# Kernel optimization log

Hardware: AMD Instinct MI355X
Metric: run time of the kernel (lower is better)

The kernel has to match this reference:

```python
import jax, jax.numpy as jnp
import numpy as np

HIDDEN_DIM = 2048
HEAD_NUM = 16
HEAD_DIM = HIDDEN_DIM // HEAD_NUM


def setup_inputs() -> dict:
    key = jax.random.key(0)
    ks = jax.random.split(key, 9)
    B, S, H = 2, 2048, HIDDEN_DIM
    scale = 1.0 / np.sqrt(H)
    X = jax.random.normal(ks[0], (B, S, H), dtype=jnp.float32)
    Wq = jax.random.normal(ks[1], (H, H), dtype=jnp.float32) * scale
    bq = jnp.zeros((H,), dtype=jnp.float32)
    Wk = jax.random.normal(ks[2], (H, H), dtype=jnp.float32) * scale
    bk = jnp.zeros((H,), dtype=jnp.float32)
    Wv = jax.random.normal(ks[3], (H, H), dtype=jnp.float32) * scale
    bv = jnp.zeros((H,), dtype=jnp.float32)
    Wo = jax.random.normal(ks[4], (H, H), dtype=jnp.float32) * scale
    bo = jnp.zeros((H,), dtype=jnp.float32)
    return {"X": X, "Wq": Wq, "bq": bq, "Wk": Wk, "bk": bk,
            "Wv": Wv, "bv": bv, "Wo": Wo, "bo": bo}


def reference(X, Wq, bq, Wk, bk, Wv, bv, Wo, bo):
    B, S, H = X.shape
    # QKV projections (nn.Linear applies x @ W.T + b; weights here stored as [in, out])
    Q = X @ Wq + bq
    K = X @ Wk + bk
    V = X @ Wv + bv
    # [B, heads, S, head_dim]
    q = Q.reshape(B, S, HEAD_NUM, HEAD_DIM).transpose(0, 2, 1, 3)
    k = K.reshape(B, S, HEAD_NUM, HEAD_DIM).transpose(0, 2, 1, 3)
    v = V.reshape(B, S, HEAD_NUM, HEAD_DIM).transpose(0, 2, 1, 3)
    scores = jnp.einsum('bhqd,bhkd->bhqk', q, k) / jnp.sqrt(jnp.float32(HEAD_DIM))
    attn = jax.nn.softmax(scores, axis=-1)  # dropout = identity in eval
    out = jnp.einsum('bhqk,bhkd->bhqd', attn, v)
    out = out.transpose(0, 2, 1, 3).reshape(B, S, H)
    return out @ Wo + bo
```

## Files before the change

### kernel.cpp

```cpp
#include <hip/hip_runtime.h>
#include <hip/hip_bf16.h>
#include <stdint.h>


#define Bc 2
#define Sc 2048
#define Hc 2048
#define NHc 16
#define Dc 128
#define Mc 4096

typedef unsigned short ushortT;
typedef float f32x4 __attribute__((ext_vector_type(4)));
typedef _Float16 f16x8 __attribute__((ext_vector_type(8)));

#define MFMAH(a, b, c) __builtin_amdgcn_mfma_f32_16x16x32_f16((a), (b), (c), 0, 0, 0)

static __device__ __forceinline__ ushortT f2h(float x) {
    _Float16 h = (_Float16)x;
    return __builtin_bit_cast(unsigned short, h);
}

static __device__ __forceinline__ void load_lds16(const ushortT* g, ushortT* l) {
    __builtin_amdgcn_global_load_lds(
        (__attribute__((address_space(1))) void*)(g),
        (__attribute__((address_space(3))) void*)(l), 16, 0, 0);
}

__global__ __launch_bounds__(256) void pack_a(
    const float* __restrict__ src, ushortT* __restrict__ dst)
{
    const int mt = blockIdx.x, kt = blockIdx.y;
    const int t = threadIdx.x;
    const int kq = t & 15;
    const int r0 = t >> 4;
    ushortT* tile = dst + ((size_t)(mt * 32 + kt)) * 8192;
#pragma unroll
    for (int rr = 0; rr < 8; ++rr) {
        const int row = r0 + rr * 16;
        const float4 v = *(const float4*)(src + (size_t)(mt * 128 + row) * Hc + kt * 64 + kq * 4);
        _Float16 h[4] = {(_Float16)v.x, (_Float16)v.y, (_Float16)v.z, (_Float16)v.w};
        const int gid = kq >> 1, halfg = kq & 1;
        const int gp = gid ^ (row & 7);
        *(uint2*)(tile + (size_t)row * 64 + gp * 8 + halfg * 4) = *(uint2*)h;
    }
}

__global__ __launch_bounds__(256) void pack_b(
    const float* __restrict__ W0, const float* __restrict__ W1,
    const float* __restrict__ W2, const float* __restrict__ W3,
    ushortT* __restrict__ dst)
{
    const int nt = blockIdx.x, kt = blockIdx.y, which = blockIdx.z;
    const float* W = (which == 0) ? W0 : (which == 1) ? W1 : (which == 2) ? W2 : W3;
    const int t = threadIdx.x;
    const int n = t & 127;
    const int g0 = (t >> 7) * 4;
    ushortT* tile = dst + (size_t)which * 4194304 + ((size_t)(nt * 32 + kt)) * 8192;
#pragma unroll
    for (int gi = 0; gi < 4; ++gi) {
        const int g = g0 + gi;
        _Float16 h[8];
#pragma unroll
        for (int j = 0; j < 8; ++j)
            h[j] = (_Float16)W[(size_t)(kt * 64 + g * 8 + j) * Hc + nt * 128 + n];
        const int gp = g ^ (n & 7);
        *(uint4*)(tile + (size_t)n * 64 + gp * 8) = *(uint4*)h;
    }
}

#define G256_PROLOGUE()                                                        \
    __shared__ __align__(16) ushortT LA[2][2][8192];                           \
    __shared__ __align__(16) ushortT LB[2][2][8192];                           \
    const int tid = threadIdx.x, wv_ = tid >> 6, lane = tid & 63;              \
    const int lane16 = lane & 15, quad = lane >> 4, quad4 = (lane >> 4) * 4;   \
    const int wr = wv_ >> 2, wc = wv_ & 3;                                     \
    f32x4 acc[8][4];                                                           \
    _Pragma("unroll") for (int i = 0; i < 8; ++i)                              \
        _Pragma("unroll") for (int j = 0; j < 4; ++j) {                        \
            acc[i][j][0] = 0.f; acc[i][j][1] = 0.f;                            \
            acc[i][j][2] = 0.f; acc[i][j][3] = 0.f; }

#define STAGE(GT, LDST) do {                                                   \
    const ushortT* g_ = (GT) + wv_ * 1024 + lane * 8;                          \
    ushortT* l_ = (LDST) + wv_ * 1024;                                         \
    load_lds16(g_, l_);                                                        \
    load_lds16(g_ + 512, l_ + 512);                                            \
} while (0)

#define RD_A(S, RB)                                                            \
    _Pragma("unroll") for (int mi = 0; mi < 4; ++mi) {                         \
        const int r_ = (RB) + mi * 16 + lane16;                                \
        _Pragma("unroll") for (int kf = 0; kf < 2; ++kf)                       \
            a[mi][kf] = *(const f16x8*)&LA[S][wr][r_ * 64 +                    \
                (((kf * 4 + quad) ^ (r_ & 7)) << 3)];                          \
    }

#define RD_B(S)                                                                \
    _Pragma("unroll") for (int nj = 0; nj < 4; ++nj) {                         \
        const int r_ = (wc & 1) * 64 + nj * 16 + lane16;                       \
        _Pragma("unroll") for (int kf = 0; kf < 2; ++kf)                       \
            b[nj][kf] = *(const f16x8*)&LB[S][wc >> 1][r_ * 64 +               \
                (((kf * 4 + quad) ^ (r_ & 7)) << 3)];                          \
    }

#define QUAD(MIB, NJB)                                                         \
    _Pragma("unroll") for (int kf = 0; kf < 2; ++kf)                           \
        _Pragma("unroll") for (int mi = 0; mi < 4; ++mi)                       \
            _Pragma("unroll") for (int nj = 0; nj < 2; ++nj)                   \
                acc[(MIB) + mi][(NJB) + nj] =                                  \
                    MFMAH(a[mi][kf], b[(NJB) + nj][kf], acc[(MIB) + mi][(NJB) + nj]);

#define PRE_MFMA()                                                             \
    __builtin_amdgcn_sched_barrier(0);                                         \
    __builtin_amdgcn_s_barrier();                                              \
    __builtin_amdgcn_sched_barrier(0);                                         \
    __builtin_amdgcn_s_setprio(1);

#define POST_MFMA()                                                            \
    __builtin_amdgcn_s_setprio(0);                                             \
    __builtin_amdgcn_sched_barrier(0);                                         \
    __builtin_amdgcn_s_barrier();                                              \
    __builtin_amdgcn_sched_barrier(0);

#define VMC6() asm volatile("s_waitcnt vmcnt(6)" ::: "memory")

#define MINS(x) ((x) < 31 ? (x) : 31)

#define G256_MAIN(AB0, AB1, BB0, BB1)                                          \
      \
    STAGE(BB0, &LB[0][0][0]); STAGE(BB1, &LB[0][1][0]);                        \
    STAGE(AB0, &LA[0][0][0]); STAGE(AB1, &LA[0][1][0]);                        \
    STAGE(BB0 + 8192, &LB[1][0][0]); STAGE(BB1 + 8192, &LB[1][1][0]);          \
    STAGE(AB0 + 8192, &LA[1][0][0]);                                           \
    VMC6();                                                                    \
    __builtin_amdgcn_sched_barrier(0);                                         \
    __builtin_amdgcn_s_barrier();                                              \
    __builtin_amdgcn_sched_barrier(0);                                         \
    _Pragma("clang loop unroll(disable)")                                      \
    for (int t = 0; t < 32; t += 2) {                                          \
        f16x8 a[4][2], b[4][2];                                                \
                                \
        RD_A(0, 0); RD_B(0);                                                   \
        STAGE(AB1 + (size_t)(t + 1) * 8192, &LA[1][1][0]);                     \
        PRE_MFMA(); QUAD(0, 0); POST_MFMA();                                   \
                                            \
        STAGE(BB0 + (size_t)MINS(t + 2) * 8192, &LB[0][0][0]);                 \
        PRE_MFMA(); QUAD(0, 2); POST_MFMA();                                   \
                                                       \
        RD_A(0, 64);                                                           \
        STAGE(BB1 + (size_t)MINS(t + 2) * 8192, &LB[0][1][0]);                 \
        PRE_MFMA(); QUAD(4, 2); POST_MFMA();                                   \
            \
        STAGE(AB0 + (size_t)MINS(t + 2) * 8192, &LA[0][0][0]);                 \
        VMC6();                                                                \
        PRE_MFMA(); QUAD(4, 0); POST_MFMA();                                   \
                                             \
        RD_A(1, 0); RD_B(1);                                                   \
        STAGE(AB1 + (size_t)MINS(t + 2) * 8192, &LA[0][1][0]);                 \
        PRE_MFMA(); QUAD(0, 0); POST_MFMA();                                   \
                                                                       \
        STAGE(BB0 + (size_t)MINS(t + 3) * 8192, &LB[1][0][0]);                 \
        PRE_MFMA(); QUAD(0, 2); POST_MFMA();                                   \
                                                                       \
        RD_A(1, 64);                                                           \
        STAGE(BB1 + (size_t)MINS(t + 3) * 8192, &LB[1][1][0]);                 \
        PRE_MFMA(); QUAD(4, 2); POST_MFMA();                                   \
                            \
        STAGE(AB0 + (size_t)MINS(t + 3) * 8192, &LA[1][0][0]);                 \
        VMC6();                                                                \
        PRE_MFMA(); QUAD(4, 0); POST_MFMA();                                   \
    }

__global__ __launch_bounds__(512, 2) void qkv_gemm256(
    const ushortT* __restrict__ Xp, const ushortT* __restrict__ Wall,
    const float* __restrict__ bq, const float* __restrict__ bk,
    const float* __restrict__ bv,
    ushortT* __restrict__ Qd, ushortT* __restrict__ Kd, ushortT* __restrict__ Vt)
{
    const int id = blockIdx.x;
    const int swz = (id & 7) * 48 + (id >> 3);
    const int mt = swz & 15;
    const int bn = swz >> 4;
    const int which = bn >> 3, bnw = bn & 7;
    const ushortT* Ab0 = Xp + (size_t)((2 * mt + 0) * 32) * 8192;
    const ushortT* Ab1 = Xp + (size_t)((2 * mt + 1) * 32) * 8192;
    const ushortT* Wp  = Wall + (size_t)which * 4194304;
    const ushortT* Bb0 = Wp + (size_t)((bnw * 2 + 0) * 32) * 8192;
    const ushortT* Bb1 = Wp + (size_t)((bnw * 2 + 1) * 32) * 8192;
    const float* bias = (which == 0) ? bq : (which == 1) ? bk : bv;

    G256_PROLOGUE();
    G256_MAIN(Ab0, Ab1, Bb0, Bb1);
    asm volatile("s_waitcnt vmcnt(0)" ::: "memory");

    const float QS = 0.08838834764831845f * 1.4426950408889634f;
#pragma unroll
    for (int nj = 0; nj < 4; ++nj) {
        const int colm = bnw * 256 + wc * 64 + nj * 16 + lane16;
        const float bb2 = bias[colm];
        const int hh = colm >> 7, dd = colm & 127;
#pragma unroll
        for (int mi = 0; mi < 8; ++mi)
#pragma unroll
            for (int r = 0; r < 4; ++r) {
                const int m = mt * 256 + wr * 128 + mi * 16 + quad4 + r;
                const int b = m >> 11, s = m & 2047;
                const float v = acc[mi][nj][r] + bb2;
                const size_t bhb = (size_t)(b * NHc + hh) * (Sc * Dc);
                if (which == 0) {
                    Qd[bhb + (size_t)s * Dc + dd] = f2h(v * QS);
                } else if (which == 1) {
                    const int t2 = s >> 6, sin_ = s & 63;
                    Kd[bhb + (size_t)t2 * 8192 + sin_ * 128 +
                       (((dd >> 3) ^ (sin_ & 7)) << 3) + (dd & 7)] = f2h(v);
                } else {
                    const int t2 = s >> 6, sin_ = s & 63;
                    Vt[bhb + (size_t)t2 * 8192 + dd * 64 +
                       (((sin_ >> 3) ^ (dd & 7)) << 3) + (sin_ & 7)] = f2h(v);
                }
            }
    }
}

__global__ __launch_bounds__(128, 2) void attn(
    const ushortT* __restrict__ Qd, const ushortT* __restrict__ Kt,
    const ushortT* __restrict__ Vt, ushortT* __restrict__ AOp)
{
    const int id = blockIdx.x;
    const int slot = id >> 3;
    const int pair = (id & 7) + ((slot >> 5) << 3);
    const int qt = slot & 31;
    const int hh = pair & 15, bb = pair >> 4;

    const ushortT* Qp  = Qd + ((size_t)(bb * NHc + hh)) * Sc * Dc;
    const ushortT* Kbh = Kt + ((size_t)(bb * NHc + hh)) * Sc * Dc;
    const ushortT* Vbh = Vt + ((size_t)(bb * NHc + hh)) * Sc * Dc;

    __shared__ __align__(16) ushortT Ks[8192];
    __shared__ __align__(16) ushortT Vs[8192];
    __shared__ __align__(16) ushortT Pbuf[2][2048];

    const int tid = threadIdx.x, wv_ = tid >> 6, lane = tid & 63;
    const int lane16 = lane & 15, quad = lane >> 4;
    const int quad8 = quad * 8, quad4 = quad * 4;
    const int s0 = qt * 64 + wv_ * 32;

    f16x8 q[2][4];
#pragma unroll
    for (int nj = 0; nj < 2; ++nj)
#pragma unroll
        for (int kf = 0; kf < 4; ++kf)
            q[nj][kf] = *(const f16x8*)(Qp + (size_t)(s0 + nj * 16 + lane16) * Dc + kf * 32 + quad8);

    f32x4 o[8][2];
#pragma unroll
    for (int dj = 0; dj < 8; ++dj)
#pragma unroll
        for (int nj = 0; nj < 2; ++nj) { o[dj][nj][0] = 0.f; o[dj][nj][1] = 0.f; o[dj][nj][2] = 0.f; o[dj][nj][3] = 0.f; }

    float m_run[2] = {-1e30f, -1e30f}, l_run[2] = {0.f, 0.f};
    ushortT* Pw = Pbuf[wv_];

    for (int nt = 0; nt < 32; ++nt) {
        const ushortT* ktile = Kbh + (size_t)nt * 8192 + wv_ * 4096;
        const ushortT* vtile = Vbh + (size_t)nt * 8192 + wv_ * 4096;
#pragma unroll
        for (int i = 0; i < 8; ++i) {
            load_lds16(ktile + i * 512 + lane * 8, Ks + wv_ * 4096 + i * 512);
            load_lds16(vtile + i * 512 + lane * 8, Vs + wv_ * 4096 + i * 512);
        }
        __syncthreads();

        f32x4 sacc[4][2];
#pragma unroll
        for (int mi = 0; mi < 4; ++mi)
#pragma unroll
            for (int nj = 0; nj < 2; ++nj) { sacc[mi][nj][0] = 0.f; sacc[mi][nj][1] = 0.f; sacc[mi][nj][2] = 0.f; sacc[mi][nj][3] = 0.f; }
#pragma unroll
        for (int kf = 0; kf < 4; ++kf) {
            f16x8 kb[4];
#pragma unroll
            for (int mi = 0; mi < 4; ++mi) {
                const int row = mi * 16 + lane16;
                kb[mi] = *(const f16x8*)&Ks[row * 128 + (((kf * 4 + quad) ^ (row & 7)) << 3)];
            }
#pragma unroll
            for (int mi = 0; mi < 4; ++mi)
#pragma unroll
                for (int nj = 0; nj < 2; ++nj)
                    sacc[mi][nj] = MFMAH(kb[mi], q[nj][kf], sacc[mi][nj]);
        }

        float alpha_[2];
#pragma unroll
        for (int nj = 0; nj < 2; ++nj) {
            float mx = sacc[0][nj][0];
#pragma unroll
            for (int mi = 0; mi < 4; ++mi)
#pragma unroll
                for (int r = 0; r < 4; ++r) mx = fmaxf(mx, sacc[mi][nj][r]);
            mx = fmaxf(mx, __shfl_xor(mx, 16));
            mx = fmaxf(mx, __shfl_xor(mx, 32));
            const float mnew = fmaxf(m_run[nj], mx);
            alpha_[nj] = exp2f(m_run[nj] - mnew);
            m_run[nj] = mnew;
            float sum = 0.f;
#pragma unroll
            for (int mi = 0; mi < 4; ++mi)
#pragma unroll
                for (int r = 0; r < 4; ++r) {
                    const float p = exp2f(sacc[mi][nj][r] - mnew);
                    sacc[mi][nj][r] = p;
                    sum += p;
                }
            sum += __shfl_xor(sum, 16);
            sum += __shfl_xor(sum, 32);
            l_run[nj] = l_run[nj] * alpha_[nj] + sum;
            const int prow = nj * 16 + lane16;
#pragma unroll
            for (int mi = 0; mi < 4; ++mi) {
                uint2 u;
                u.x = (uint32_t)f2h(sacc[mi][nj][0]) | ((uint32_t)f2h(sacc[mi][nj][1]) << 16);
                u.y = (uint32_t)f2h(sacc[mi][nj][2]) | ((uint32_t)f2h(sacc[mi][nj][3]) << 16);
                const int g = mi * 2 + (quad >> 1);
                *(uint2*)&Pw[prow * 64 + ((g ^ (prow & 7)) << 3) + (quad & 1) * 4] = u;
            }
        }

#pragma unroll
        for (int dj = 0; dj < 8; ++dj)
#pragma unroll
            for (int nj = 0; nj < 2; ++nj) {
                const float av = alpha_[nj];
                o[dj][nj][0] *= av; o[dj][nj][1] *= av;
                o[dj][nj][2] *= av; o[dj][nj][3] *= av;
            }

#pragma unroll
        for (int kf2 = 0; kf2 < 2; ++kf2) {
            f16x8 pb[2];
#pragma unroll
            for (int nj = 0; nj < 2; ++nj) {
                const int row = nj * 16 + lane16;
                pb[nj] = *(const f16x8*)&Pw[row * 64 + (((kf2 * 4 + quad) ^ (row & 7)) << 3)];
            }
#pragma unroll
            for (int dj = 0; dj < 8; ++dj) {
                const int row = dj * 16 + lane16;
                const f16x8 vb = *(const f16x8*)&Vs[row * 64 + (((kf2 * 4 + quad) ^ (row & 7)) << 3)];
#pragma unroll
                for (int nj = 0; nj < 2; ++nj)
                    o[dj][nj] = MFMAH(vb, pb[nj], o[dj][nj]);
            }
        }
        __syncthreads();
    }

#pragma unroll
    for (int nj = 0; nj < 2; ++nj) {
        const float inv = 1.f / l_run[nj];
        const int m = bb * Sc + qt * 64 + wv_ * 32 + nj * 16 + lane16;
        const int mtile = m >> 7, rin = m & 127;
#pragma unroll
        for (int dj = 0; dj < 8; ++dj) {
            const int ktile = hh * 2 + (dj >> 2);
            const int cin0 = (dj & 3) * 16 + quad4;
            const int g = cin0 >> 3, e0 = cin0 & 7;
            uint2 u;
            u.x = (uint32_t)f2h(o[dj][nj][0] * inv) | ((uint32_t)f2h(o[dj][nj][1] * inv) << 16);
            u.y = (uint32_t)f2h(o[dj][nj][2] * inv) | ((uint32_t)f2h(o[dj][nj][3] * inv) << 16);
            *(uint2*)&AOp[((size_t)(mtile * 32 + ktile)) * 8192 + rin * 64 +
                          ((g ^ (rin & 7)) << 3) + e0] = u;
        }
    }
}

__global__ __launch_bounds__(512, 2) void out_gemm256(
    const ushortT* __restrict__ AOp, const ushortT* __restrict__ Wop,
    const float* __restrict__ bo, float* __restrict__ out)
{
    const int id = blockIdx.x;
    const int swz = (id & 7) * 16 + (id >> 3);
    const int mt = swz & 15;
    const int bn = swz >> 4;
    const ushortT* Ab0 = AOp + (size_t)((2 * mt + 0) * 32) * 8192;
    const ushortT* Ab1 = AOp + (size_t)((2 * mt + 1) * 32) * 8192;
    const ushortT* Bb0 = Wop + (size_t)((bn * 2 + 0) * 32) * 8192;
    const ushortT* Bb1 = Wop + (size_t)((bn * 2 + 1) * 32) * 8192;

    G256_PROLOGUE();
    G256_MAIN(Ab0, Ab1, Bb0, Bb1);
    asm volatile("s_waitcnt vmcnt(0)" ::: "memory");

#pragma unroll
    for (int nj = 0; nj < 4; ++nj) {
        const int col = bn * 256 + wc * 64 + nj * 16 + lane16;
        const float bb2 = bo[col];
#pragma unroll
        for (int mi = 0; mi < 8; ++mi)
#pragma unroll
            for (int r = 0; r < 4; ++r) {
                const int m = mt * 256 + wr * 128 + mi * 16 + quad4 + r;
                out[(size_t)m * Hc + col] = acc[mi][nj][r] + bb2;
            }
    }
}

extern "C" void kernel_launch(void* const* d_in, const int* in_sizes, int n_in,
                              void* d_out, int out_size, void* d_ws, size_t ws_size,
                              hipStream_t stream) {
    (void)in_sizes; (void)n_in; (void)out_size; (void)ws_size;

    const float* X  = (const float*)d_in[0];
    const float* Wq = (const float*)d_in[1];
    const float* bq = (const float*)d_in[2];
    const float* Wk = (const float*)d_in[3];
    const float* bk = (const float*)d_in[4];
    const float* Wv = (const float*)d_in[5];
    const float* bv = (const float*)d_in[6];
    const float* Wo = (const float*)d_in[7];
    const float* bo = (const float*)d_in[8];
    float* out = (float*)d_out;

    ushortT* ws = (ushortT*)d_ws;
    const size_t E = (size_t)Mc * Hc;
    const size_t WE = (size_t)Hc * Hc;
    ushortT* Xp   = ws;
    ushortT* Wall = Xp + E;
    ushortT* Qd   = Wall + 4 * WE;
    ushortT* Kd   = Qd + E;
    ushortT* Vtp  = Kd + E;
    ushortT* AOp  = Vtp + E;

    pack_a<<<dim3(32, 32), 256, 0, stream>>>(X, Xp);
    pack_b<<<dim3(16, 32, 4), 256, 0, stream>>>(Wq, Wk, Wv, Wo, Wall);
    qkv_gemm256<<<dim3(384), 512, 0, stream>>>(Xp, Wall, bq, bk, bv, Qd, Kd, Vtp);
    attn<<<dim3(1024), 128, 0, stream>>>(Qd, Kd, Vtp, AOp);
    out_gemm256<<<dim3(128), 512, 0, stream>>>(AOp, Wall + 3 * WE, bo, out);
}
```

Before: 501.6 us.

## Use 128x128 single-buffered GEMM for output projection and precompute LDS offsets

The output projection moves from the 256x256 double-buffered 8-wave kernel (128 blocks) to a simpler 128x128 4-wave kernel with a 16x32 grid (512 blocks). The aim is better occupancy and CU coverage on a machine with many CUs, at the cost of a single-buffered loop that syncs twice per k-step with no load/compute overlap. The 256 GEMM macros now precompute swizzled LDS read offsets and base pointers to cut per-iteration address arithmetic. The QKV epilogue hoists per-row index math and packs V-transposed stores into 8-byte writes.

Result: faster. 458.0 us (-8.7%).

```diff
diff --git a/kernel.cpp b/kernel.cpp
--- a/kernel.cpp
+++ b/kernel.cpp
@@ -69,40 +69,91 @@
     }
 }
 
+#define GEMM_PROLOGUE()                                                        \
+    __shared__ __align__(16) ushortT As[8192], Bs[8192];                       \
+    const int tid = threadIdx.x, wv_ = tid >> 6, lane = tid & 63;              \
+    const int lane16 = lane & 15, quad = lane >> 4;                            \
+    const int quad4 = quad * 4;                                                \
+    const int wm = (wv_ & 1) * 64, wn = (wv_ >> 1) * 64;                       \
+    int aoff[4][2], boff[4][2];                                                \
+    _Pragma("unroll") for (int mi = 0; mi < 4; ++mi)                           \
+        _Pragma("unroll") for (int kf = 0; kf < 2; ++kf) {                     \
+            const int ra = wm + mi * 16 + lane16;                              \
+            aoff[mi][kf] = ra * 64 + (((kf * 4 + quad) ^ (ra & 7)) << 3);      \
+            const int rb = wn + mi * 16 + lane16;                              \
+            boff[mi][kf] = rb * 64 + (((kf * 4 + quad) ^ (rb & 7)) << 3);      \
+        }                                                                      \
+    f32x4 acc[4][4];                                                           \
+    _Pragma("unroll") for (int i = 0; i < 4; ++i)                              \
+        _Pragma("unroll") for (int j = 0; j < 4; ++j) {                        \
+            acc[i][j][0] = 0.f; acc[i][j][1] = 0.f;                            \
+            acc[i][j][2] = 0.f; acc[i][j][3] = 0.f; }                          \
+    ushortT* asd = &As[wv_ * 2048];                                            \
+    ushortT* bsd = &Bs[wv_ * 2048];
+
+#define GEMM_KLOOP(at, bt)                                                     \
+    for (int kt2 = 0; kt2 < 32; ++kt2) {                                       \
+        _Pragma("unroll") for (int i = 0; i < 4; ++i) {                        \
+            load_lds16(at + i * 512 + lane * 8, asd + i * 512);                \
+            load_lds16(bt + i * 512 + lane * 8, bsd + i * 512);                \
+        }                                                                      \
+        at += 8192; bt += 8192;                                                \
+        __syncthreads();                                                       \
+        _Pragma("unroll") for (int kf = 0; kf < 2; ++kf) {                     \
+            f16x8 a[4], b[4];                                                  \
+            _Pragma("unroll") for (int mi = 0; mi < 4; ++mi)                   \
+                a[mi] = *(const f16x8*)&As[aoff[mi][kf]];                      \
+            _Pragma("unroll") for (int nj = 0; nj < 4; ++nj)                   \
+                b[nj] = *(const f16x8*)&Bs[boff[nj][kf]];                      \
+            _Pragma("unroll") for (int nj = 0; nj < 4; ++nj)                   \
+                _Pragma("unroll") for (int mi = 0; mi < 4; ++mi)               \
+                    acc[mi][nj] = MFMAH(a[mi], b[nj], acc[mi][nj]);            \
+        }                                                                      \
+        __syncthreads();                                                       \
+    }
+
 #define G256_PROLOGUE()                                                        \
     __shared__ __align__(16) ushortT LA[2][2][8192];                           \
     __shared__ __align__(16) ushortT LB[2][2][8192];                           \
     const int tid = threadIdx.x, wv_ = tid >> 6, lane = tid & 63;              \
     const int lane16 = lane & 15, quad = lane >> 4, quad4 = (lane >> 4) * 4;   \
     const int wr = wv_ >> 2, wc = wv_ & 3;                                     \
+    const ushortT* LAr = &LA[0][0][0] + wr * 8192;                             \
+    const ushortT* LBr = &LB[0][0][0] + (wc >> 1) * 8192;                      \
+    int oA[2][4][2], oB[4][2];                                                 \
+    _Pragma("unroll") for (int h = 0; h < 2; ++h)                              \
+        _Pragma("unroll") for (int mi = 0; mi < 4; ++mi)                       \
+            _Pragma("unroll") for (int kf = 0; kf < 2; ++kf) {                 \
+                const int r_ = h * 64 + mi * 16 + lane16;                      \
+                oA[h][mi][kf] = r_ * 64 + (((kf * 4 + quad) ^ (r_ & 7)) << 3); \
+            }                                                                  \
+    _Pragma("unroll") for (int nj = 0; nj < 4; ++nj)                           \
+        _Pragma("unroll") for (int kf = 0; kf < 2; ++kf) {                     \
+            const int r_ = (wc & 1) * 64 + nj * 16 + lane16;                   \
+            oB[nj][kf] = r_ * 64 + (((kf * 4 + quad) ^ (r_ & 7)) << 3);        \
+        }                                                                      \
     f32x4 acc[8][4];                                                           \
     _Pragma("unroll") for (int i = 0; i < 8; ++i)                              \
         _Pragma("unroll") for (int j = 0; j < 4; ++j) {                        \
             acc[i][j][0] = 0.f; acc[i][j][1] = 0.f;                            \
             acc[i][j][2] = 0.f; acc[i][j][3] = 0.f; }
 
-#define STAGE(GT, LDST) do {                                                   \
-    const ushortT* g_ = (GT) + wv_ * 1024 + lane * 8;                          \
-    ushortT* l_ = (LDST) + wv_ * 1024;                                         \
+#define STAGE(SRC, STEP, DST) do {                                             \
+    const ushortT* g_ = (SRC) + (size_t)(STEP) * 8192;                         \
+    ushortT* l_ = (DST) + wv_ * 1024;                                          \
     load_lds16(g_, l_);                                                        \
     load_lds16(g_ + 512, l_ + 512);                                            \
 } while (0)
 
-#define RD_A(S, RB)                                                            \
-    _Pragma("unroll") for (int mi = 0; mi < 4; ++mi) {                         \
-        const int r_ = (RB) + mi * 16 + lane16;                                \
+#define RD_A(S, H)                                                             \
+    _Pragma("unroll") for (int mi = 0; mi < 4; ++mi)                           \
         _Pragma("unroll") for (int kf = 0; kf < 2; ++kf)                       \
-            a[mi][kf] = *(const f16x8*)&LA[S][wr][r_ * 64 +                    \
-                (((kf * 4 + quad) ^ (r_ & 7)) << 3)];                          \
-    }
+            a[mi][kf] = *(const f16x8*)&LAr[(S) * 16384 + oA[H][mi][kf]];
 
 #define RD_B(S)                                                                \
-    _Pragma("unroll") for (int nj = 0; nj < 4; ++nj) {                         \
-        const int r_ = (wc & 1) * 64 + nj * 16 + lane16;                       \
+    _Pragma("unroll") for (int nj = 0; nj < 4; ++nj)                           \
         _Pragma("unroll") for (int kf = 0; kf < 2; ++kf)                       \
-            b[nj][kf] = *(const f16x8*)&LB[S][wc >> 1][r_ * 64 +               \
-                (((kf * 4 + quad) ^ (r_ & 7)) << 3)];                          \
-    }
+            b[nj][kf] = *(const f16x8*)&LBr[(S) * 16384 + oB[nj][kf]];
 
 #define QUAD(MIB, NJB)                                                         \
     _Pragma("unroll") for (int kf = 0; kf < 2; ++kf)                           \
@@ -128,11 +179,15 @@
 #define MINS(x) ((x) < 31 ? (x) : 31)
 
 #define G256_MAIN(AB0, AB1, BB0, BB1)                                          \
+    const ushortT* sA0 = (AB0) + wv_ * 1024 + lane * 8;                        \
+    const ushortT* sA1 = (AB1) + wv_ * 1024 + lane * 8;                        \
+    const ushortT* sB0 = (BB0) + wv_ * 1024 + lane * 8;                        \
+    const ushortT* sB1 = (BB1) + wv_ * 1024 + lane * 8;                        \
       \
-    STAGE(BB0, &LB[0][0][0]); STAGE(BB1, &LB[0][1][0]);                        \
-    STAGE(AB0, &LA[0][0][0]); STAGE(AB1, &LA[0][1][0]);                        \
-    STAGE(BB0 + 8192, &LB[1][0][0]); STAGE(BB1 + 8192, &LB[1][1][0]);          \
-    STAGE(AB0 + 8192, &LA[1][0][0]);                                           \
+    STAGE(sB0, 0, &LB[0][0][0]); STAGE(sB1, 0, &LB[0][1][0]);                  \
+    STAGE(sA0, 0, &LA[0][0][0]); STAGE(sA1, 0, &LA[0][1][0]);                  \
+    STAGE(sB0, 1, &LB[1][0][0]); STAGE(sB1, 1, &LB[1][1][0]);                  \
+    STAGE(sA0, 1, &LA[1][0][0]);                                               \
     VMC6();                                                                    \
     __builtin_amdgcn_sched_barrier(0);                                         \
     __builtin_amdgcn_s_barrier();                                              \
@@ -142,32 +197,32 @@
         f16x8 a[4][2], b[4][2];                                                \
                                 \
         RD_A(0, 0); RD_B(0);                                                   \
-        STAGE(AB1 + (size_t)(t + 1) * 8192, &LA[1][1][0]);                     \
+        STAGE(sA1, t + 1, &LA[1][1][0]);                                       \
         PRE_MFMA(); QUAD(0, 0); POST_MFMA();                                   \
                                             \
-        STAGE(BB0 + (size_t)MINS(t + 2) * 8192, &LB[0][0][0]);                 \
+        STAGE(sB0, MINS(t + 2), &LB[0][0][0]);                                 \
         PRE_MFMA(); QUAD(0, 2); POST_MFMA();                                   \
                                                        \
-        RD_A(0, 64);                                                           \
-        STAGE(BB1 + (size_t)MINS(t + 2) * 8192, &LB[0][1][0]);                 \
+        RD_A(0, 1);                                                            \
+        STAGE(sB1, MINS(t + 2), &LB[0][1][0]);                                 \
         PRE_MFMA(); QUAD(4, 2); POST_MFMA();                                   \
             \
-        STAGE(AB0 + (size_t)MINS(t + 2) * 8192, &LA[0][0][0]);                 \
+        STAGE(sA0, MINS(t + 2), &LA[0][0][0]);                                 \
         VMC6();                                                                \
         PRE_MFMA(); QUAD(4, 0); POST_MFMA();                                   \
                                              \
         RD_A(1, 0); RD_B(1);                                                   \
-        STAGE(AB1 + (size_t)MINS(t + 2) * 8192, &LA[0][1][0]);                 \
+        STAGE(sA1, MINS(t + 2), &LA[0][1][0]);                                 \
         PRE_MFMA(); QUAD(0, 0); POST_MFMA();                                   \
                                                                        \
-        STAGE(BB0 + (size_t)MINS(t + 3) * 8192, &LB[1][0][0]);                 \
+        STAGE(sB0, MINS(t + 3), &LB[1][0][0]);                                 \
         PRE_MFMA(); QUAD(0, 2); POST_MFMA();                                   \
                                                                        \
-        RD_A(1, 64);                                                           \
-        STAGE(BB1 + (size_t)MINS(t + 3) * 8192, &LB[1][1][0]);                 \
+        RD_A(1, 1);                                                            \
+        STAGE(sB1, MINS(t + 3), &LB[1][1][0]);                                 \
         PRE_MFMA(); QUAD(4, 2); POST_MFMA();                                   \
                             \
-        STAGE(AB0 + (size_t)MINS(t + 3) * 8192, &LA[1][0][0]);                 \
+        STAGE(sA0, MINS(t + 3), &LA[1][0][0]);                                 \
         VMC6();                                                                \
         PRE_MFMA(); QUAD(4, 0); POST_MFMA();                                   \
     }
@@ -201,25 +256,36 @@
         const float bb2 = bias[colm];
         const int hh = colm >> 7, dd = colm & 127;
 #pragma unroll
-        for (int mi = 0; mi < 8; ++mi)
-#pragma unroll
-            for (int r = 0; r < 4; ++r) {
-                const int m = mt * 256 + wr * 128 + mi * 16 + quad4 + r;
-                const int b = m >> 11, s = m & 2047;
-                const float v = acc[mi][nj][r] + bb2;
-                const size_t bhb = (size_t)(b * NHc + hh) * (Sc * Dc);
-                if (which == 0) {
-                    Qd[bhb + (size_t)s * Dc + dd] = f2h(v * QS);
-                } else if (which == 1) {
+        for (int mi = 0; mi < 8; ++mi) {
+            const int m0 = mt * 256 + wr * 128 + mi * 16 + quad4;
+            const int b = m0 >> 11, s0_ = m0 & 2047;
+            const size_t bhb = (size_t)(b * NHc + hh) * (Sc * Dc);
+            if (which == 0) {
+#pragma unroll
+                for (int r = 0; r < 4; ++r) {
+                    const float v = acc[mi][nj][r] + bb2;
+                    Qd[bhb + (size_t)(s0_ + r) * Dc + dd] = f2h(v * QS);
+                }
+            } else if (which == 1) {
+#pragma unroll
+                for (int r = 0; r < 4; ++r) {
+                    const float v = acc[mi][nj][r] + bb2;
+                    const int s = s0_ + r;
                     const int t2 = s >> 6, sin_ = s & 63;
                     Kd[bhb + (size_t)t2 * 8192 + sin_ * 128 +
                        (((dd >> 3) ^ (sin_ & 7)) << 3) + (dd & 7)] = f2h(v);
-                } else {
-                    const int t2 = s >> 6, sin_ = s & 63;
-                    Vt[bhb + (size_t)t2 * 8192 + dd * 64 +
-                       (((sin_ >> 3) ^ (dd & 7)) << 3) + (sin_ & 7)] = f2h(v);
                 }
-            }
+            } else {
+                const int t2 = s0_ >> 6, sin0 = s0_ & 63;
+                uint2 u;
+                u.x = (uint32_t)f2h(acc[mi][nj][0] + bb2) |
+                      ((uint32_t)f2h(acc[mi][nj][1] + bb2) << 16);
+                u.y = (uint32_t)f2h(acc[mi][nj][2] + bb2) |
+                      ((uint32_t)f2h(acc[mi][nj][3] + bb2) << 16);
+                *(uint2*)&Vt[bhb + (size_t)t2 * 8192 + dd * 64 +
+                             (((sin0 >> 3) ^ (dd & 7)) << 3) + (sin0 & 7)] = u;
+            }
+        }
     }
 }
 
@@ -376,33 +442,29 @@
     }
 }
 
-__global__ __launch_bounds__(512, 2) void out_gemm256(
+__global__ __launch_bounds__(256) void out_gemm(
     const ushortT* __restrict__ AOp, const ushortT* __restrict__ Wop,
     const float* __restrict__ bo, float* __restrict__ out)
 {
-    const int id = blockIdx.x;
-    const int swz = (id & 7) * 16 + (id >> 3);
-    const int mt = swz & 15;
-    const int bn = swz >> 4;
-    const ushortT* Ab0 = AOp + (size_t)((2 * mt + 0) * 32) * 8192;
-    const ushortT* Ab1 = AOp + (size_t)((2 * mt + 1) * 32) * 8192;
-    const ushortT* Bb0 = Wop + (size_t)((bn * 2 + 0) * 32) * 8192;
-    const ushortT* Bb1 = Wop + (size_t)((bn * 2 + 1) * 32) * 8192;
-
-    G256_PROLOGUE();
-    G256_MAIN(Ab0, Ab1, Bb0, Bb1);
-    asm volatile("s_waitcnt vmcnt(0)" ::: "memory");
+    const int nt = blockIdx.x;
+    const int mt = blockIdx.y;
+
+    GEMM_PROLOGUE();
+
+    const ushortT* at = AOp + (size_t)(mt * 32) * 8192 + wv_ * 2048;
+    const ushortT* bt = Wop + (size_t)(nt * 32) * 8192 + wv_ * 2048;
+    GEMM_KLOOP(at, bt);
 
 #pragma unroll
     for (int nj = 0; nj < 4; ++nj) {
-        const int col = bn * 256 + wc * 64 + nj * 16 + lane16;
-        const float bb2 = bo[col];
-#pragma unroll
-        for (int mi = 0; mi < 8; ++mi)
+        const int col = nt * 128 + wn + nj * 16 + lane16;
+        const float bb = bo[col];
+#pragma unroll
+        for (int mi = 0; mi < 4; ++mi)
 #pragma unroll
             for (int r = 0; r < 4; ++r) {
-                const int m = mt * 256 + wr * 128 + mi * 16 + quad4 + r;
-                out[(size_t)m * Hc + col] = acc[mi][nj][r] + bb2;
+                const int m = mt * 128 + wm + mi * 16 + quad4 + r;
+                out[(size_t)m * Hc + col] = acc[mi][nj][r] + bb;
             }
     }
 }
@@ -437,5 +499,5 @@
     pack_b<<<dim3(16, 32, 4), 256, 0, stream>>>(Wq, Wk, Wv, Wo, Wall);
     qkv_gemm256<<<dim3(384), 512, 0, stream>>>(Xp, Wall, bq, bk, bv, Qd, Kd, Vtp);
     attn<<<dim3(1024), 128, 0, stream>>>(Qd, Kd, Vtp, AOp);
-    out_gemm256<<<dim3(128), 512, 0, stream>>>(AOp, Wall + 3 * WE, bo, out);
-}
+    out_gemm<<<dim3(16, 32), 256, 0, stream>>>(AOp, Wall + 3 * WE, bo, out);
+}
```
